# Optimization experiments

Hardware: AMD Instinct MI355X
Metric: run time of the kernel (lower is better)

## Reference

```python
import jax, jax.numpy as jnp
import numpy as np

LBASE = 256
L1_BASE = LBASE // 2 + 1   # 129
LPA = 128
L1_PA = LPA + 1            # 129
L2 = 16
L2_HALF = L2 // 2          # 8
L3 = 64
LOUTPUT = L3 + LPA + LBASE // 2  # 320
MAX_PLY = 60
COUNT = 6
BUCKET_SIZE = MAX_PLY // COUNT   # 10
B = 262144


def setup_inputs() -> dict:
    key = jax.random.key(0)
    ks = jax.random.split(key, 12)
    def w(k, shape, fan_in):
        bound = 1.0 / np.sqrt(fan_in)
        return jax.random.uniform(k, shape, jnp.float32, -bound, bound)
    return {
        "x_base": jax.random.uniform(ks[0], (B, LBASE // 2), jnp.float32),
        "x_pa": jax.random.uniform(ks[1], (B, LPA), jnp.float32),
        "mobility": jax.random.uniform(ks[2], (B, 1), jnp.float32),
        "ply": jax.random.randint(ks[3], (B,), 0, MAX_PLY),
        "W1b": w(ks[4], (COUNT, L2_HALF, L1_BASE), L1_BASE),
        "b1b": w(ks[5], (COUNT, L2_HALF), L1_BASE),
        "W1pa": w(ks[6], (COUNT, L2_HALF, L1_PA), L1_PA),
        "b1pa": w(ks[7], (COUNT, L2_HALF), L1_PA),
        "W2": w(ks[8], (COUNT, L3, L2 * 2), L2 * 2),
        "b2": w(ks[9], (COUNT, L3), L2 * 2),
        "Wout": w(ks[10], (COUNT, 1, LOUTPUT), LOUTPUT),
        "bout": jnp.zeros((COUNT, 1), jnp.float32),  # bias zeroed in __init__
    }


def _stacked_linear(x, W, b, idx):
    # per-sample bucket selection: x (B,I), W (C,O,I), b (C,O), idx (B,)
    return jnp.einsum("bi,boi->bo", x, W[idx]) + b[idx]


def reference(x_base, x_pa, mobility, ply, W1b, b1b, W1pa, b1pa, W2, b2, Wout, bout):
    idx = ply // BUCKET_SIZE                                   # (B,)
    mob = jnp.minimum(mobility * (7.0 / 255.0), 1.0)           # clamp max only
    xb = jnp.concatenate([x_base, mob], axis=1)                # (B,129)
    xpa = jnp.concatenate([x_pa, mob], axis=1)                 # (B,129)
    l1 = jnp.concatenate([
        _stacked_linear(xb, W1b, b1b, idx),
        _stacked_linear(xpa, W1pa, b1pa, idx),
    ], axis=1)                                                 # (B,16)
    l1_sq = jnp.square(l1) * (255.0 / 256.0)
    l1c = jnp.clip(jnp.concatenate([l1_sq, l1], axis=1), 0.0, 1.0)  # (B,32)
    l2x = _stacked_linear(l1c, W2, b2, idx)                    # (B,64)
    l2x = jnp.square(jnp.clip(l2x, 0.0, 1.0)) * (255.0 / 256.0)
    feats = jnp.concatenate([l2x, x_base, x_pa], axis=1)       # (B,320)
    return _stacked_linear(feats, Wout, bout, idx)             # (B,1)
```

## Files before the change

### kernel.cpp

```cpp
#include <hip/hip_runtime.h>


#define NB 6

typedef _Float16 h2 __attribute__((ext_vector_type(2)));
typedef _Float16 h8 __attribute__((ext_vector_type(8)));
typedef float f4 __attribute__((ext_vector_type(4)));

__device__ __forceinline__ h2 pk2(float x, float y) {
    return __builtin_bit_cast(h2, __builtin_amdgcn_cvt_pkrtz(x, y));
}

__device__ __forceinline__ h8 pack8(const float4 a, const float4 b) {
    h2 p0 = pk2(a.x, a.y), p1 = pk2(a.z, a.w);
    h2 p2 = pk2(b.x, b.y), p3 = pk2(b.z, b.w);
    h8 r;
    r[0] = p0[0]; r[1] = p0[1]; r[2] = p1[0]; r[3] = p1[1];
    r[4] = p2[0]; r[5] = p2[1]; r[6] = p3[0]; r[7] = p3[1];
    return r;
}

__device__ __forceinline__ float actv(float v) {
    float u = fminf(fmaxf(v, 0.0f), 1.0f);
    return u * u * (255.0f / 256.0f);
}

__global__ __launch_bounds__(1024, 1)
void layerstacks_mfma(const float* __restrict__ x_base,
                      const float* __restrict__ x_pa,
                      const float* __restrict__ mobility,
                      const int*   __restrict__ ply,
                      const float* __restrict__ W1b,
                      const float* __restrict__ b1b,
                      const float* __restrict__ W1pa,
                      const float* __restrict__ b1pa,
                      const float* __restrict__ W2,
                      const float* __restrict__ b2,
                      const float* __restrict__ Wout,
                      const float* __restrict__ bout,
                      float* __restrict__ out)
{
    __shared__ __align__(16) _Float16 sW1[NB][2][4][4][9][8];
    __shared__ __align__(16) _Float16 sW2[NB][4][4][16][8];
    __shared__ float sWo0[NB][64];
    __shared__ float sB2[NB][64];
    __shared__ float sB1[NB][4][8];
    __shared__ float sBout[NB];
    __shared__ float sMob[1024];
    __shared__ int   sList[1120];
    __shared__ __align__(16) char sL1[16 * 1280];
    __shared__ int sCnt[8], sCur[8], sTb[72];
    __shared__ int sNt;

    const int tid   = threadIdx.x;
    const int lane  = tid & 63;
    const int w     = tid >> 6;
    const int gbase = blockIdx.x << 10;

    if (tid < 8) { sCnt[tid] = 0; }

    for (int e = tid; e < NB * 2 * 4 * 4 * 9 * 8; e += 1024) {
        int i = e & 7;
        int rest = e >> 3;
        int n = rest % 9;   rest /= 9;
        int kb = rest & 3;  rest >>= 2;
        int t = rest & 3;   rest >>= 2;
        int st = rest & 1;
        int b = rest >> 1;
        int k = t * 32 + kb * 8 + i;
        float v;
        if (n < 8) {
            const float* Wx = st ? W1pa : W1b;
            v = Wx[b * 1032 + n * 129 + k];
        } else {
            v = st ? Wout[b * 320 + 192 + k] : Wout[b * 320 + 64 + k];
        }
        sW1[b][st][t][kb][n][i] = (_Float16)v;
    }
    for (int e = tid; e < NB * 4 * 4 * 16 * 8; e += 1024) {
        int i = e & 7;
        int j = (e >> 3) & 15;
        int kb = (e >> 7) & 3;
        int T = (e >> 9) & 3;
        int b = e >> 11;
        int n = T * 16 + j;
        int k = kb * 8 + i;
        int u = k >> 1;
        int colw = (k & 1) ? (16 + u) : u;
        sW2[b][T][kb][j][i] = (_Float16)W2[b * 2048 + n * 32 + colw];
    }
    for (int e = tid; e < NB * 64; e += 1024) {
        int b = e >> 6, n = e & 63;
        sWo0[b][n] = Wout[b * 320 + n];
        sB2[b][n]  = b2[e];
    }
    if (tid < NB * 4 * 8) {
        int n = tid & 7, which = (tid >> 3) & 3, b = tid >> 5;
        float v;
        if (which == 0)      v = b1b[b * 8 + n];
        else if (which == 1) v = b1pa[b * 8 + n];
        else if (which == 2) v = W1b [b * 1032 + n * 129 + 128];
        else                 v = W1pa[b * 1032 + n * 129 + 128];
        sB1[b][which][n] = v;
    }
    if (tid < NB) sBout[tid] = bout[tid];
    sMob[tid] = fminf(mobility[gbase + tid] * (7.0f / 255.0f), 1.0f);
    for (int e = tid; e < 1120; e += 1024) sList[e] = -1;

    const int bb = ply[gbase + tid] / 10;
    __syncthreads();

    #pragma unroll
    for (int b = 0; b < NB; ++b) {
        unsigned long long mk = __ballot(bb == b);
        if (bb == b) {
            int lead = __ffsll((long long)mk) - 1;
            if (lane == lead) atomicAdd(&sCnt[b], __popcll(mk));
        }
    }
    __syncthreads();

    if (tid == 0) {
        int off = 0, tt = 0;
        for (int b = 0; b < NB; ++b) {
            sCur[b] = off;
            int ntl = (sCnt[b] + 15) >> 4;
            for (int q = 0; q < ntl; ++q) sTb[tt++] = b;
            off += ntl << 4;
        }
        sNt = tt;
    }
    __syncthreads();

    #pragma unroll
    for (int b = 0; b < NB; ++b) {
        unsigned long long mk = __ballot(bb == b);
        if (bb == b) {
            int lead = __ffsll((long long)mk) - 1;
            int pfx = __popcll(mk & ((1ull << lane) - 1ull));
            int base = 0;
            if (lane == lead) base = atomicAdd(&sCur[b], __popcll(mk));
            base = __shfl(base, lead);
            sList[base + pfx] = tid;
        }
    }
    __syncthreads();

    const int ntiles = sNt;
    const int col = lane & 15;
    const int qd  = lane >> 4;
    char* lb = sL1 + w * 1280;

    for (int tl = w; tl < ntiles; tl += 16) {
        const int bkt = sTb[tl];
        const int t16 = tl << 4;

        const int sl0 = sList[t16 + qd * 4 + 0];
        const int sl1 = sList[t16 + qd * 4 + 1];
        const int sl2 = sList[t16 + qd * 4 + 2];
        const int sl3 = sList[t16 + qd * 4 + 3];
        const float mob0 = (sl0 >= 0) ? sMob[sl0 & 1023] : 0.0f;
        const float mob1 = (sl1 >= 0) ? sMob[sl1 & 1023] : 0.0f;
        const float mob2 = (sl2 >= 0) ? sMob[sl2 & 1023] : 0.0f;
        const float mob3 = (sl3 >= 0) ? sMob[sl3 & 1023] : 0.0f;
        int sA = sList[t16 + col];
        if (sA < 0) sA = sList[t16];

        const int c7 = col & 7;
        const bool a8 = (col < 8);
        const float bb1 = sB1[bkt][0][c7], bp1 = sB1[bkt][1][c7];
        const float mwb = sB1[bkt][2][c7], mwp = sB1[bkt][3][c7];
        f4 cb, cp;
        cb[0] = a8 ? bb1 + mwb * mob0 : 0.0f;
        cb[1] = a8 ? bb1 + mwb * mob1 : 0.0f;
        cb[2] = a8 ? bb1 + mwb * mob2 : 0.0f;
        cb[3] = a8 ? bb1 + mwb * mob3 : 0.0f;
        cp[0] = a8 ? bp1 + mwp * mob0 : 0.0f;
        cp[1] = a8 ? bp1 + mwp * mob1 : 0.0f;
        cp[2] = a8 ? bp1 + mwp * mob2 : 0.0f;
        cp[3] = a8 ? bp1 + mwp * mob3 : 0.0f;

        const int ncl = a8 ? col : 8;
        const float* xbrow = x_base + (size_t)(gbase + sA) * 128;
        const float* xprow = x_pa   + (size_t)(gbase + sA) * 128;

        #pragma unroll
        for (int t4 = 0; t4 < 4; ++t4) {
            const float4 a0 = *(const float4*)(xbrow + t4 * 32 + qd * 8);
            const float4 a1 = *(const float4*)(xbrow + t4 * 32 + qd * 8 + 4);
            const float4 p0 = *(const float4*)(xprow + t4 * 32 + qd * 8);
            const float4 p1 = *(const float4*)(xprow + t4 * 32 + qd * 8 + 4);
            const h8 xa = pack8(a0, a1);
            const h8 xp = pack8(p0, p1);
            const h8 wa = *(const h8*)&sW1[bkt][0][t4][qd][ncl][0];
            const h8 wp = *(const h8*)&sW1[bkt][1][t4][qd][ncl][0];
            cb = __builtin_amdgcn_mfma_f32_16x16x32_f16(xa, wa, cb, 0, 0, 0);
            cp = __builtin_amdgcn_mfma_f32_16x16x32_f16(xp, wp, cp, 0, 0, 0);
        }

        if (col < 8) {
            #pragma unroll
            for (int r = 0; r < 4; ++r) {
                const int row = qd * 4 + r;
                float v = cb[r];
                *(h2*)(lb + row * 80 + col * 4) =
                    pk2(fminf(v * v * (255.0f / 256.0f), 1.0f),
                        fminf(fmaxf(v, 0.0f), 1.0f));
                v = cp[r];
                *(h2*)(lb + row * 80 + 32 + col * 4) =
                    pk2(fminf(v * v * (255.0f / 256.0f), 1.0f),
                        fminf(fmaxf(v, 0.0f), 1.0f));
            }
        } else if (col == 8) {
            #pragma unroll
            for (int r = 0; r < 4; ++r) {
                const int row = qd * 4 + r;
                *(float*)(lb + row * 80 + 64) = cb[r];
                *(float*)(lb + row * 80 + 68) = cp[r];
            }
        }

        const h8 a2 = *(const h8*)(lb + col * 80 + qd * 16);
        const float s0 = sB2[bkt][col];
        const float s1 = sB2[bkt][16 + col];
        const float s2 = sB2[bkt][32 + col];
        const float s3 = sB2[bkt][48 + col];
        f4 c20 = {s0, s0, s0, s0};
        f4 c21 = {s1, s1, s1, s1};
        f4 c22 = {s2, s2, s2, s2};
        f4 c23 = {s3, s3, s3, s3};
        c20 = __builtin_amdgcn_mfma_f32_16x16x32_f16(a2, *(const h8*)&sW2[bkt][0][qd][col][0], c20, 0, 0, 0);
        c21 = __builtin_amdgcn_mfma_f32_16x16x32_f16(a2, *(const h8*)&sW2[bkt][1][qd][col][0], c21, 0, 0, 0);
        c22 = __builtin_amdgcn_mfma_f32_16x16x32_f16(a2, *(const h8*)&sW2[bkt][2][qd][col][0], c22, 0, 0, 0);
        c23 = __builtin_amdgcn_mfma_f32_16x16x32_f16(a2, *(const h8*)&sW2[bkt][3][qd][col][0], c23, 0, 0, 0);

        const float wo0 = sWo0[bkt][col];
        const float wo1 = sWo0[bkt][16 + col];
        const float wo2 = sWo0[bkt][32 + col];
        const float wo3 = sWo0[bkt][48 + col];
        float p0 = actv(c20[0]) * wo0 + actv(c21[0]) * wo1 + actv(c22[0]) * wo2 + actv(c23[0]) * wo3;
        float p1 = actv(c20[1]) * wo0 + actv(c21[1]) * wo1 + actv(c22[1]) * wo2 + actv(c23[1]) * wo3;
        float p2 = actv(c20[2]) * wo0 + actv(c21[2]) * wo1 + actv(c22[2]) * wo2 + actv(c23[2]) * wo3;
        float p3 = actv(c20[3]) * wo0 + actv(c21[3]) * wo1 + actv(c22[3]) * wo2 + actv(c23[3]) * wo3;
        #pragma unroll
        for (int m = 1; m < 16; m <<= 1) {
            p0 += __shfl_xor(p0, m, 64);
            p1 += __shfl_xor(p1, m, 64);
            p2 += __shfl_xor(p2, m, 64);
            p3 += __shfl_xor(p3, m, 64);
        }

        if (col == 0) {
            const float bo = sBout[bkt];
            if (sl0 >= 0)
                out[gbase + sl0] = bo + *(const float*)(lb + (qd * 4 + 0) * 80 + 64)
                                      + *(const float*)(lb + (qd * 4 + 0) * 80 + 68) + p0;
            if (sl1 >= 0)
                out[gbase + sl1] = bo + *(const float*)(lb + (qd * 4 + 1) * 80 + 64)
                                      + *(const float*)(lb + (qd * 4 + 1) * 80 + 68) + p1;
            if (sl2 >= 0)
                out[gbase + sl2] = bo + *(const float*)(lb + (qd * 4 + 2) * 80 + 64)
                                      + *(const float*)(lb + (qd * 4 + 2) * 80 + 68) + p2;
            if (sl3 >= 0)
                out[gbase + sl3] = bo + *(const float*)(lb + (qd * 4 + 3) * 80 + 64)
                                      + *(const float*)(lb + (qd * 4 + 3) * 80 + 68) + p3;
        }
    }
}

extern "C" void kernel_launch(void* const* d_in, const int* in_sizes, int n_in,
                              void* d_out, int out_size, void* d_ws, size_t ws_size,
                              hipStream_t stream) {
    const float* x_base   = (const float*)d_in[0];
    const float* x_pa     = (const float*)d_in[1];
    const float* mobility = (const float*)d_in[2];
    const int*   ply      = (const int*)d_in[3];
    const float* W1b      = (const float*)d_in[4];
    const float* b1b      = (const float*)d_in[5];
    const float* W1pa     = (const float*)d_in[6];
    const float* b1pa     = (const float*)d_in[7];
    const float* W2       = (const float*)d_in[8];
    const float* b2       = (const float*)d_in[9];
    const float* Wout     = (const float*)d_in[10];
    const float* bout     = (const float*)d_in[11];
    float* out = (float*)d_out;

    const int B = in_sizes[3];
    const int blocks = B >> 10;
    layerstacks_mfma<<<blocks, 1024, 0, stream>>>(
        x_base, x_pa, mobility, ply, W1b, b1b, W1pa, b1pa, W2, b2, Wout, bout, out);
}
```

Before: 63.28 us.

## Split each tile across wave pairs and halve samples per block

Each 16-sample tile is now processed by two waves, one for the base features and one for the PA features. Each wave does half of the layer-2 columns, and partial sums are combined through LDS with block-wide barriers. Blocks now cover 512 samples instead of 1024, so there are twice as many blocks, and mobility is read directly from global memory instead of being staged in shared memory. This is meant to raise parallelism and memory-level concurrency per tile and shorten each wave's dependent MFMA chain. In exchange it adds three __syncthreads per round and repeats the weight staging work in twice as many blocks.

```diff
diff --git a/kernel.cpp b/kernel.cpp
--- a/kernel.cpp
+++ b/kernel.cpp
@@ -2,6 +2,9 @@
 
 
 #define NB 6
+#define BT 1024
+#define SPB 512
+#define MAXT (SPB / 16 + NB)
 
 typedef _Float16 h2 __attribute__((ext_vector_type(2)));
 typedef _Float16 h8 __attribute__((ext_vector_type(8)));
@@ -25,7 +28,7 @@
     return u * u * (255.0f / 256.0f);
 }
 
-__global__ __launch_bounds__(1024, 1)
+__global__ __launch_bounds__(BT, 8)
 void layerstacks_mfma(const float* __restrict__ x_base,
                       const float* __restrict__ x_pa,
                       const float* __restrict__ mobility,
@@ -46,20 +49,21 @@
     __shared__ float sB2[NB][64];
     __shared__ float sB1[NB][4][8];
     __shared__ float sBout[NB];
-    __shared__ float sMob[1024];
-    __shared__ int   sList[1120];
-    __shared__ __align__(16) char sL1[16 * 1280];
-    __shared__ int sCnt[8], sCur[8], sTb[72];
+    __shared__ int   sList[SPB + NB * 16];
+    __shared__ __align__(16) char sL1[8 * 1280];
+    __shared__ int sCnt[8], sCur[8], sTb[MAXT + 2];
     __shared__ int sNt;
 
     const int tid   = threadIdx.x;
     const int lane  = tid & 63;
     const int w     = tid >> 6;
-    const int gbase = blockIdx.x << 10;
+    const int slot  = w >> 1;
+    const int h     = w & 1;
+    const int gbase = blockIdx.x * SPB;
 
     if (tid < 8) { sCnt[tid] = 0; }
 
-    for (int e = tid; e < NB * 2 * 4 * 4 * 9 * 8; e += 1024) {
+    for (int e = tid; e < NB * 2 * 4 * 4 * 9 * 8; e += BT) {
         int i = e & 7;
         int rest = e >> 3;
         int n = rest % 9;   rest /= 9;
@@ -77,7 +81,7 @@
         }
         sW1[b][st][t][kb][n][i] = (_Float16)v;
     }
-    for (int e = tid; e < NB * 4 * 4 * 16 * 8; e += 1024) {
+    for (int e = tid; e < NB * 4 * 4 * 16 * 8; e += BT) {
         int i = e & 7;
         int j = (e >> 3) & 15;
         int kb = (e >> 7) & 3;
@@ -89,7 +93,7 @@
         int colw = (k & 1) ? (16 + u) : u;
         sW2[b][T][kb][j][i] = (_Float16)W2[b * 2048 + n * 32 + colw];
     }
-    for (int e = tid; e < NB * 64; e += 1024) {
+    for (int e = tid; e < NB * 64; e += BT) {
         int b = e >> 6, n = e & 63;
         sWo0[b][n] = Wout[b * 320 + n];
         sB2[b][n]  = b2[e];
@@ -104,10 +108,9 @@
         sB1[b][which][n] = v;
     }
     if (tid < NB) sBout[tid] = bout[tid];
-    sMob[tid] = fminf(mobility[gbase + tid] * (7.0f / 255.0f), 1.0f);
-    for (int e = tid; e < 1120; e += 1024) sList[e] = -1;
-
-    const int bb = ply[gbase + tid] / 10;
+    for (int e = tid; e < SPB + NB * 16; e += BT) sList[e] = -1;
+
+    const int bb = (tid < SPB) ? (ply[gbase + tid] / 10) : -1;
     __syncthreads();
 
     #pragma unroll
@@ -147,124 +150,124 @@
     __syncthreads();
 
     const int ntiles = sNt;
+    const int nrounds = (ntiles + 7) >> 3;
     const int col = lane & 15;
     const int qd  = lane >> 4;
-    char* lb = sL1 + w * 1280;
-
-    for (int tl = w; tl < ntiles; tl += 16) {
-        const int bkt = sTb[tl];
-        const int t16 = tl << 4;
-
-        const int sl0 = sList[t16 + qd * 4 + 0];
-        const int sl1 = sList[t16 + qd * 4 + 1];
-        const int sl2 = sList[t16 + qd * 4 + 2];
-        const int sl3 = sList[t16 + qd * 4 + 3];
-        const float mob0 = (sl0 >= 0) ? sMob[sl0 & 1023] : 0.0f;
-        const float mob1 = (sl1 >= 0) ? sMob[sl1 & 1023] : 0.0f;
-        const float mob2 = (sl2 >= 0) ? sMob[sl2 & 1023] : 0.0f;
-        const float mob3 = (sl3 >= 0) ? sMob[sl3 & 1023] : 0.0f;
-        int sA = sList[t16 + col];
-        if (sA < 0) sA = sList[t16];
-
-        const int c7 = col & 7;
-        const bool a8 = (col < 8);
-        const float bb1 = sB1[bkt][0][c7], bp1 = sB1[bkt][1][c7];
-        const float mwb = sB1[bkt][2][c7], mwp = sB1[bkt][3][c7];
-        f4 cb, cp;
-        cb[0] = a8 ? bb1 + mwb * mob0 : 0.0f;
-        cb[1] = a8 ? bb1 + mwb * mob1 : 0.0f;
-        cb[2] = a8 ? bb1 + mwb * mob2 : 0.0f;
-        cb[3] = a8 ? bb1 + mwb * mob3 : 0.0f;
-        cp[0] = a8 ? bp1 + mwp * mob0 : 0.0f;
-        cp[1] = a8 ? bp1 + mwp * mob1 : 0.0f;
-        cp[2] = a8 ? bp1 + mwp * mob2 : 0.0f;
-        cp[3] = a8 ? bp1 + mwp * mob3 : 0.0f;
-
-        const int ncl = a8 ? col : 8;
-        const float* xbrow = x_base + (size_t)(gbase + sA) * 128;
-        const float* xprow = x_pa   + (size_t)(gbase + sA) * 128;
-
-        #pragma unroll
-        for (int t4 = 0; t4 < 4; ++t4) {
-            const float4 a0 = *(const float4*)(xbrow + t4 * 32 + qd * 8);
-            const float4 a1 = *(const float4*)(xbrow + t4 * 32 + qd * 8 + 4);
-            const float4 p0 = *(const float4*)(xprow + t4 * 32 + qd * 8);
-            const float4 p1 = *(const float4*)(xprow + t4 * 32 + qd * 8 + 4);
-            const h8 xa = pack8(a0, a1);
-            const h8 xp = pack8(p0, p1);
-            const h8 wa = *(const h8*)&sW1[bkt][0][t4][qd][ncl][0];
-            const h8 wp = *(const h8*)&sW1[bkt][1][t4][qd][ncl][0];
-            cb = __builtin_amdgcn_mfma_f32_16x16x32_f16(xa, wa, cb, 0, 0, 0);
-            cp = __builtin_amdgcn_mfma_f32_16x16x32_f16(xp, wp, cp, 0, 0, 0);
-        }
-
-        if (col < 8) {
+    char* lb = sL1 + slot * 1280;
+
+    for (int rnd = 0; rnd < nrounds; ++rnd) {
+        const int tl = rnd * 8 + slot;
+        const bool active = (tl < ntiles);
+        int bkt = 0, t16 = 0;
+
+        if (active) {
+            bkt = sTb[tl];
+            t16 = tl << 4;
+
+            const int sl0 = sList[t16 + qd * 4 + 0];
+            const int sl1 = sList[t16 + qd * 4 + 1];
+            const int sl2 = sList[t16 + qd * 4 + 2];
+            const int sl3 = sList[t16 + qd * 4 + 3];
+            int sA = sList[t16 + col];
+            if (sA < 0) sA = sList[t16];
+
+            const float* xr = (h ? x_pa : x_base) + (size_t)(gbase + sA) * 128 + qd * 8;
+            const float4 x00 = *(const float4*)(xr + 0);
+            const float4 x01 = *(const float4*)(xr + 4);
+            const float4 x10 = *(const float4*)(xr + 32);
+            const float4 x11 = *(const float4*)(xr + 36);
+            const float4 x20 = *(const float4*)(xr + 64);
+            const float4 x21 = *(const float4*)(xr + 68);
+            const float4 x30 = *(const float4*)(xr + 96);
+            const float4 x31 = *(const float4*)(xr + 100);
+
+            const int c7 = col & 7;
+            const bool a8 = (col < 8);
+            const int ncl = a8 ? col : 8;
+
+            const h8 w0 = *(const h8*)&sW1[bkt][h][0][qd][ncl][0];
+            const h8 w1 = *(const h8*)&sW1[bkt][h][1][qd][ncl][0];
+            const h8 w2f = *(const h8*)&sW1[bkt][h][2][qd][ncl][0];
+            const h8 w3 = *(const h8*)&sW1[bkt][h][3][qd][ncl][0];
+
+            const float mob0 = (sl0 >= 0) ? fminf(mobility[gbase + sl0] * (7.0f / 255.0f), 1.0f) : 0.0f;
+            const float mob1 = (sl1 >= 0) ? fminf(mobility[gbase + sl1] * (7.0f / 255.0f), 1.0f) : 0.0f;
+            const float mob2 = (sl2 >= 0) ? fminf(mobility[gbase + sl2] * (7.0f / 255.0f), 1.0f) : 0.0f;
+            const float mob3 = (sl3 >= 0) ? fminf(mobility[gbase + sl3] * (7.0f / 255.0f), 1.0f) : 0.0f;
+            const float b1v = sB1[bkt][h][c7];
+            const float mwv = sB1[bkt][2 + h][c7];
+
+            f4 c;
+            c[0] = a8 ? b1v + mwv * mob0 : 0.0f;
+            c[1] = a8 ? b1v + mwv * mob1 : 0.0f;
+            c[2] = a8 ? b1v + mwv * mob2 : 0.0f;
+            c[3] = a8 ? b1v + mwv * mob3 : 0.0f;
+
+            c = __builtin_amdgcn_mfma_f32_16x16x32_f16(pack8(x00, x01), w0, c, 0, 0, 0);
+            c = __builtin_amdgcn_mfma_f32_16x16x32_f16(pack8(x10, x11), w1, c, 0, 0, 0);
+            c = __builtin_amdgcn_mfma_f32_16x16x32_f16(pack8(x20, x21), w2f, c, 0, 0, 0);
+            c = __builtin_amdgcn_mfma_f32_16x16x32_f16(pack8(x30, x31), w3, c, 0, 0, 0);
+
+            if (col < 8) {
+                #pragma unroll
+                for (int r = 0; r < 4; ++r) {
+                    const int row = qd * 4 + r;
+                    const float v = c[r];
+                    *(h2*)(lb + row * 80 + h * 32 + col * 4) =
+                        pk2(fminf(v * v * (255.0f / 256.0f), 1.0f),
+                            fminf(fmaxf(v, 0.0f), 1.0f));
+                }
+            } else if (col == 8) {
+                #pragma unroll
+                for (int r = 0; r < 4; ++r)
+                    *(float*)(lb + (qd * 4 + r) * 80 + 64 + h * 4) = c[r];
+            }
+        }
+        __syncthreads();
+
+        if (active) {
+            const h8 a2 = *(const h8*)(lb + col * 80 + qd * 16);
+            const int T0 = 2 * h, T1 = 2 * h + 1;
+            const float s0 = sB2[bkt][T0 * 16 + col];
+            const float s1 = sB2[bkt][T1 * 16 + col];
+            f4 c20 = {s0, s0, s0, s0};
+            f4 c21 = {s1, s1, s1, s1};
+            c20 = __builtin_amdgcn_mfma_f32_16x16x32_f16(a2, *(const h8*)&sW2[bkt][T0][qd][col][0], c20, 0, 0, 0);
+            c21 = __builtin_amdgcn_mfma_f32_16x16x32_f16(a2, *(const h8*)&sW2[bkt][T1][qd][col][0], c21, 0, 0, 0);
+
+            const float wo0 = sWo0[bkt][T0 * 16 + col];
+            const float wo1 = sWo0[bkt][T1 * 16 + col];
+            float p0 = actv(c20[0]) * wo0 + actv(c21[0]) * wo1;
+            float p1 = actv(c20[1]) * wo0 + actv(c21[1]) * wo1;
+            float p2 = actv(c20[2]) * wo0 + actv(c21[2]) * wo1;
+            float p3 = actv(c20[3]) * wo0 + actv(c21[3]) * wo1;
             #pragma unroll
-            for (int r = 0; r < 4; ++r) {
-                const int row = qd * 4 + r;
-                float v = cb[r];
-                *(h2*)(lb + row * 80 + col * 4) =
-                    pk2(fminf(v * v * (255.0f / 256.0f), 1.0f),
-                        fminf(fmaxf(v, 0.0f), 1.0f));
-                v = cp[r];
-                *(h2*)(lb + row * 80 + 32 + col * 4) =
-                    pk2(fminf(v * v * (255.0f / 256.0f), 1.0f),
-                        fminf(fmaxf(v, 0.0f), 1.0f));
-            }
-        } else if (col == 8) {
-            #pragma unroll
-            for (int r = 0; r < 4; ++r) {
-                const int row = qd * 4 + r;
-                *(float*)(lb + row * 80 + 64) = cb[r];
-                *(float*)(lb + row * 80 + 68) = cp[r];
-            }
-        }
-
-        const h8 a2 = *(const h8*)(lb + col * 80 + qd * 16);
-        const float s0 = sB2[bkt][col];
-        const float s1 = sB2[bkt][16 + col];
-        const float s2 = sB2[bkt][32 + col];
-        const float s3 = sB2[bkt][48 + col];
-        f4 c20 = {s0, s0, s0, s0};
-        f4 c21 = {s1, s1, s1, s1};
-        f4 c22 = {s2, s2, s2, s2};
-        f4 c23 = {s3, s3, s3, s3};
-        c20 = __builtin_amdgcn_mfma_f32_16x16x32_f16(a2, *(const h8*)&sW2[bkt][0][qd][col][0], c20, 0, 0, 0);
-        c21 = __builtin_amdgcn_mfma_f32_16x16x32_f16(a2, *(const h8*)&sW2[bkt][1][qd][col][0], c21, 0, 0, 0);
-        c22 = __builtin_amdgcn_mfma_f32_16x16x32_f16(a2, *(const h8*)&sW2[bkt][2][qd][col][0], c22, 0, 0, 0);
-        c23 = __builtin_amdgcn_mfma_f32_16x16x32_f16(a2, *(const h8*)&sW2[bkt][3][qd][col][0], c23, 0, 0, 0);
-
-        const float wo0 = sWo0[bkt][col];
-        const float wo1 = sWo0[bkt][16 + col];
-        const float wo2 = sWo0[bkt][32 + col];
-        const float wo3 = sWo0[bkt][48 + col];
-        float p0 = actv(c20[0]) * wo0 + actv(c21[0]) * wo1 + actv(c22[0]) * wo2 + actv(c23[0]) * wo3;
-        float p1 = actv(c20[1]) * wo0 + actv(c21[1]) * wo1 + actv(c22[1]) * wo2 + actv(c23[1]) * wo3;
-        float p2 = actv(c20[2]) * wo0 + actv(c21[2]) * wo1 + actv(c22[2]) * wo2 + actv(c23[2]) * wo3;
-        float p3 = actv(c20[3]) * wo0 + actv(c21[3]) * wo1 + actv(c22[3]) * wo2 + actv(c23[3]) * wo3;
-        #pragma unroll
-        for (int m = 1; m < 16; m <<= 1) {
-            p0 += __shfl_xor(p0, m, 64);
-            p1 += __shfl_xor(p1, m, 64);
-            p2 += __shfl_xor(p2, m, 64);
-            p3 += __shfl_xor(p3, m, 64);
-        }
-
-        if (col == 0) {
-            const float bo = sBout[bkt];
-            if (sl0 >= 0)
-                out[gbase + sl0] = bo + *(const float*)(lb + (qd * 4 + 0) * 80 + 64)
-                                      + *(const float*)(lb + (qd * 4 + 0) * 80 + 68) + p0;
-            if (sl1 >= 0)
-                out[gbase + sl1] = bo + *(const float*)(lb + (qd * 4 + 1) * 80 + 64)
-                                      + *(const float*)(lb + (qd * 4 + 1) * 80 + 68) + p1;
-            if (sl2 >= 0)
-                out[gbase + sl2] = bo + *(const float*)(lb + (qd * 4 + 2) * 80 + 64)
-                                      + *(const float*)(lb + (qd * 4 + 2) * 80 + 68) + p2;
-            if (sl3 >= 0)
-                out[gbase + sl3] = bo + *(const float*)(lb + (qd * 4 + 3) * 80 + 64)
-                                      + *(const float*)(lb + (qd * 4 + 3) * 80 + 68) + p3;
-        }
+            for (int m = 1; m < 16; m <<= 1) {
+                p0 += __shfl_xor(p0, m, 64);
+                p1 += __shfl_xor(p1, m, 64);
+                p2 += __shfl_xor(p2, m, 64);
+                p3 += __shfl_xor(p3, m, 64);
+            }
+            if (col == 0) {
+                *(float*)(lb + (qd * 4 + 0) * 80 + 72 + h * 4) = p0;
+                *(float*)(lb + (qd * 4 + 1) * 80 + 72 + h * 4) = p1;
+                *(float*)(lb + (qd * 4 + 2) * 80 + 72 + h * 4) = p2;
+                *(float*)(lb + (qd * 4 + 3) * 80 + 72 + h * 4) = p3;
+            }
+        }
+        __syncthreads();
+
+        if (active && h == 0 && lane < 16) {
+            const int row = lane;
+            const int sl = sList[t16 + row];
+            if (sl >= 0) {
+                const char* rp = lb + row * 80;
+                out[gbase + sl] = sBout[bkt]
+                                + *(const float*)(rp + 64) + *(const float*)(rp + 68)
+                                + *(const float*)(rp + 72) + *(const float*)(rp + 76);
+            }
+        }
+        __syncthreads();
     }
 }
 
@@ -286,7 +289,7 @@
     float* out = (float*)d_out;
 
     const int B = in_sizes[3];
-    const int blocks = B >> 10;
-    layerstacks_mfma<<<blocks, 1024, 0, stream>>>(
+    const int blocks = B / SPB;
+    layerstacks_mfma<<<blocks, BT, 0, stream>>>(
         x_base, x_pa, mobility, ply, W1b, b1b, W1pa, b1pa, W2, b2, Wout, bout, out);
 }
```

New measurement: 95.13 us. 1.5x slower.
